# Kernel tuning notes

Hardware: AMD Instinct MI355X
Metric: run time of the kernel (lower is better)

Reference implementation:

```python
import jax, jax.numpy as jnp
import numpy as np

H = 512  # hidden_size
D = 512  # input_size
EPS = 1e-5  # torch LayerNorm default


def _ln(u, g, b):
    # LayerNorm over last dim, biased variance (matches torch)
    m = jnp.mean(u, axis=-1, keepdims=True)
    v = jnp.mean(jnp.square(u - m), axis=-1, keepdims=True)
    return (u - m) * jax.lax.rsqrt(v + EPS) * g + b


def _cell(x_t, h, c, W, b, ln_g, ln_b):
    # gates: [B, 4H] from concat([x_t, h]) @ W.T + b
    z = jnp.concatenate([x_t, h], axis=-1) @ W.T + b
    i_raw, f_raw, g_raw, o_raw = jnp.split(z, 4, axis=-1)
    i = jax.nn.sigmoid(_ln(i_raw, ln_g[0], ln_b[0]))
    f = jax.nn.sigmoid(_ln(f_raw, ln_g[1], ln_b[1]))
    g = jnp.tanh(_ln(g_raw, ln_g[2], ln_b[2]))
    o = jax.nn.sigmoid(_ln(o_raw, ln_g[3], ln_b[3]))
    c_new = f * c + i * g
    h_new = o * jnp.tanh(_ln(c_new, ln_g[4], ln_b[4]))
    return h_new, c_new


def setup_inputs() -> dict:
    key = jax.random.key(0)
    ks = jax.random.split(key, 5)
    B, T = 64, 1024
    x = jax.random.normal(ks[0], (B, T, D), dtype=jnp.float32)
    W0 = jax.random.normal(ks[1], (4 * H, D + H), dtype=jnp.float32) * 0.02
    b0 = jnp.zeros((4 * H,), jnp.float32)
    W1 = jax.random.normal(ks[2], (4 * H, H + H), dtype=jnp.float32) * 0.02
    b1 = jnp.zeros((4 * H,), jnp.float32)
    ln_g0 = jnp.ones((5, H), jnp.float32)
    ln_b0 = jnp.zeros((5, H), jnp.float32)
    ln_g1 = jnp.ones((5, H), jnp.float32)
    ln_b1 = jnp.zeros((5, H), jnp.float32)
    hw_W = jax.random.normal(ks[3], (H, H), dtype=jnp.float32) * 0.02
    hw_b = jnp.zeros((H,), jnp.float32)
    return {"x": x, "W0": W0, "b0": b0, "ln_g0": ln_g0, "ln_b0": ln_b0,
            "W1": W1, "b1": b1, "ln_g1": ln_g1, "ln_b1": ln_b1,
            "hw_W": hw_W, "hw_b": hw_b}


def reference(x, W0, b0, ln_g0, ln_b0, W1, b1, ln_g1, ln_b1, hw_W, hw_b):
    B, T, _ = x.shape
    h0 = jnp.zeros((B, H), x.dtype)
    c0 = jnp.zeros((B, H), x.dtype)
    h1 = jnp.zeros((B, H), x.dtype)
    c1 = jnp.zeros((B, H), x.dtype)

    def step(carry, x_t):
        h0, c0, h1, c1 = carry
        h0n, c0n = _cell(x_t, h0, c0, W0, b0, ln_g0, ln_b0)
        # dropout=0.0 -> identity between layers
        h1n, c1n = _cell(h0n, h1, c1, W1, b1, ln_g1, ln_b1)
        # highway: gate computed from h_in (= layer-0 output)
        g = jax.nn.sigmoid(h0n @ hw_W.T + hw_b)
        out_t = g * h1n + (1.0 - g) * h0n
        return (h0n, c0n, h1n, c1n), out_t

    xs = jnp.transpose(x, (1, 0, 2))  # [T, B, D]
    (h0, c0, h1, c1), outs = jax.lax.scan(step, (h0, c0, h1, c1), xs)
    output = jnp.transpose(outs, (1, 0, 2))  # [B, T, H]
    h_n = jnp.stack([h0, h1], axis=0)  # [num_layers, B, H]
    c_n = jnp.stack([c0, c1], axis=0)
    return output, h_n, c_n
```

## Files before the change

### kernel.cpp

```cpp
#include <hip/hip_runtime.h>

#define TT 1024
#define BB 64
#define HH 512
#define DD 512
#define NBLK 256
#define NTHR 256
#define NGRP 8

#define W0T4_OFF 0
#define W1T4_OFF 2097152
#define H0_OFF   4194304
#define H1_OFF   4227072
#define Z0_OFF   4259840
#define Z1_OFF   4390912
#define HWZ_OFF  4521984
#define FLG_OFF  4554752

__device__ __forceinline__ float ldg_cg(const float* p) {
    return __hip_atomic_load(p, __ATOMIC_RELAXED, __HIP_MEMORY_SCOPE_AGENT);
}
__device__ __forceinline__ void stg_cg(float* p, float v) {
    __hip_atomic_store(p, v, __ATOMIC_RELAXED, __HIP_MEMORY_SCOPE_AGENT);
}
__device__ __forceinline__ float4 ldg_cg4(const float* p) {
    const unsigned long long* q = (const unsigned long long*)p;
    unsigned long long a = __hip_atomic_load(q,     __ATOMIC_RELAXED, __HIP_MEMORY_SCOPE_AGENT);
    unsigned long long b = __hip_atomic_load(q + 1, __ATOMIC_RELAXED, __HIP_MEMORY_SCOPE_AGENT);
    float4 v;
    ((unsigned long long*)&v)[0] = a;
    ((unsigned long long*)&v)[1] = b;
    return v;
}
__device__ __forceinline__ unsigned ldg_cgu(const unsigned* p) {
    return __hip_atomic_load(p, __ATOMIC_RELAXED, __HIP_MEMORY_SCOPE_AGENT);
}

__device__ __forceinline__ void group_barrier(unsigned* gfl, unsigned tgt, int slot, int tid)
{
    __syncthreads();
    if (tid == 0)
        __hip_atomic_store(&gfl[slot * 32], tgt, __ATOMIC_RELEASE, __HIP_MEMORY_SCOPE_AGENT);
    if (tid < 32) {
        while (ldg_cgu(&gfl[tid * 32]) < tgt) __builtin_amdgcn_s_sleep(1);
    }
    __syncthreads();
}

__global__ void ln_lstm_init_kernel(const float* __restrict__ W0, const float* __restrict__ W1,
                                    float* __restrict__ ws)
{
    const int stride = gridDim.x * blockDim.x;
    const int idx = blockIdx.x * blockDim.x + threadIdx.x;
    for (int i = idx; i < 2048 * 256; i += stride) {
        const int R = i & 2047, kq = i >> 11;
        const float4 v0 = *(const float4*)&W0[(size_t)R * 1024 + kq * 4];
        const float4 v1 = *(const float4*)&W1[(size_t)R * 1024 + kq * 4];
        *(float4*)&ws[W0T4_OFF + ((size_t)kq * 2048 + R) * 4] = v0;
        *(float4*)&ws[W1T4_OFF + ((size_t)kq * 2048 + R) * 4] = v1;
    }
    for (int i = idx; i < 65536; i += stride) ws[H0_OFF + i] = 0.f;
    unsigned* uw = (unsigned*)ws;
    for (int i = idx; i < 8192; i += stride) uw[FLG_OFF + i] = 0u;
}

__device__ __forceinline__ void gemv_k4(const float4* __restrict__ wt, const float* __restrict__ inT,
                                        float* __restrict__ zr, int bq, int r, int Rrow,
                                        float& z0, float& z1)
{
    float a[8];
#pragma unroll
    for (int i = 0; i < 8; ++i) a[i] = 0.f;
    const float4* wp = wt + (size_t)(bq * 64) * 2048 + Rrow;
    const float* ib = inT + bq * 256;
    for (int c = 0; c < 4; ++c) {
        float4 w[16];
#pragma unroll
        for (int i = 0; i < 16; ++i) w[i] = wp[(size_t)(c * 16 + i) * 2048];
#pragma unroll
        for (int i = 0; i < 16; ++i) {
            const int kk = c * 64 + i * 4;
#pragma unroll
            for (int bi = 0; bi < 8; ++bi) {
                const float4 iv = *(const float4*)&ib[bi * 1024 + kk];
                a[bi] += w[i].x * iv.x + w[i].y * iv.y + w[i].z * iv.z + w[i].w * iv.w;
            }
        }
    }
#pragma unroll
    for (int bi = 0; bi < 8; ++bi) zr[bq * 512 + bi * 64 + r] = a[bi];
    __syncthreads();
    z0 = 0.f; z1 = 0.f;
#pragma unroll
    for (int w2 = 0; w2 < 4; ++w2) {
        z0 += zr[w2 * 512 + bq * 64 + r];
        z1 += zr[w2 * 512 + (bq + 4) * 64 + r];
    }
}

__device__ __forceinline__ void block_reduce8(float v[8], float* sred, int tid)
{
#pragma unroll
    for (int off = 32; off > 0; off >>= 1)
#pragma unroll
        for (int k = 0; k < 8; ++k) v[k] += __shfl_down(v[k], off, 64);
    __syncthreads();
    if ((tid & 63) == 0) {
        const int wv = tid >> 6;
#pragma unroll
        for (int k = 0; k < 8; ++k) sred[k * 4 + wv] = v[k];
    }
    __syncthreads();
#pragma unroll
    for (int k = 0; k < 8; ++k)
        v[k] = sred[k * 4 + 0] + sred[k * 4 + 1] + sred[k * 4 + 2] + sred[k * 4 + 3];
}
__device__ __forceinline__ void block_reduce2(float& s1, float& s2, float* sred, int tid)
{
#pragma unroll
    for (int off = 32; off > 0; off >>= 1) {
        s1 += __shfl_down(s1, off, 64);
        s2 += __shfl_down(s2, off, 64);
    }
    __syncthreads();
    if ((tid & 63) == 0) {
        const int wv = tid >> 6;
        sred[wv] = s1; sred[4 + wv] = s2;
    }
    __syncthreads();
    s1 = sred[0] + sred[1] + sred[2] + sred[3];
    s2 = sred[4] + sred[5] + sred[6] + sred[7];
}

__device__ __forceinline__ void cell(const float* __restrict__ zg, const float* __restrict__ gb,
                                     const float* __restrict__ lng, const float* __restrict__ lnb,
                                     float cc[2], float* __restrict__ hws_b, float hv[2],
                                     float* sred, int tid)
{
    float z[4][2];
#pragma unroll
    for (int g = 0; g < 4; ++g) {
        z[g][0] = ldg_cg(zg + g * 512 + tid)       + gb[g * 512 + tid];
        z[g][1] = ldg_cg(zg + g * 512 + tid + 256) + gb[g * 512 + tid + 256];
    }
    float st[8];
#pragma unroll
    for (int g = 0; g < 4; ++g) {
        st[g]     = z[g][0] + z[g][1];
        st[4 + g] = z[g][0] * z[g][0] + z[g][1] * z[g][1];
    }
    block_reduce8(st, sred, tid);
    float act[4][2];
#pragma unroll
    for (int g = 0; g < 4; ++g) {
        const float mu = st[g] * (1.f / 512.f);
        const float rs = rsqrtf(st[4 + g] * (1.f / 512.f) - mu * mu + 1e-5f);
#pragma unroll
        for (int e = 0; e < 2; ++e) {
            const int j = tid + e * 256;
            const float a = (z[g][e] - mu) * rs * lng[g * 512 + j] + lnb[g * 512 + j];
            act[g][e] = (g == 2) ? tanhf(a) : 1.f / (1.f + expf(-a));
        }
    }
    float cn[2];
#pragma unroll
    for (int e = 0; e < 2; ++e) {
        cn[e] = act[1][e] * cc[e] + act[0][e] * act[2][e];
        cc[e] = cn[e];
    }
    float s1 = cn[0] + cn[1];
    float s2 = cn[0] * cn[0] + cn[1] * cn[1];
    block_reduce2(s1, s2, sred, tid);
    const float mu = s1 * (1.f / 512.f);
    const float rs = rsqrtf(s2 * (1.f / 512.f) - mu * mu + 1e-5f);
#pragma unroll
    for (int e = 0; e < 2; ++e) {
        const int j = tid + e * 256;
        const float h = act[3][e] * tanhf((cn[e] - mu) * rs * lng[2048 + j] + lnb[2048 + j]);
        stg_cg(hws_b + j, h);
        hv[e] = h;
    }
}

__global__ __launch_bounds__(NTHR, 1)
void LayerNormLSTMStack_55508157333865_kernel(
    const float* __restrict__ x,
    const float* __restrict__ W0, const float* __restrict__ gb0,
    const float* __restrict__ lng0, const float* __restrict__ lnb0,
    const float* __restrict__ W1, const float* __restrict__ gb1,
    const float* __restrict__ lng1, const float* __restrict__ lnb1,
    const float* __restrict__ hwW, const float* __restrict__ hwb,
    float* __restrict__ out, float* __restrict__ ws)
{
    __shared__ __align__(16) float inT[8 * 1024];
    __shared__ __align__(16) float zr[4 * 512];
    __shared__ float sred[32];
    __shared__ float hwred[256];

    const int tid = threadIdx.x;
    const int grp = blockIdx.x >> 5;
    const int bg  = blockIdx.x & 31;
    const int bb0 = grp * 8;
    const int r = tid & 63, bq = tid >> 6;
    const int R0 = bg * 64;

    const float4* w0t = (const float4*)(ws + W0T4_OFF);
    const float4* w1t = (const float4*)(ws + W1T4_OFF);
    float* h0ws  = ws + H0_OFF;
    float* h1ws  = ws + H1_OFF;
    float* z0g   = ws + Z0_OFF + grp * 16384;
    float* z1g   = ws + Z1_OFF + grp * 16384;
    float* hwzg  = ws + HWZ_OFF + grp * 4096;
    unsigned* gfl = (unsigned*)ws + FLG_OFF + grp * 1024;

    float c0[2] = {0.f, 0.f}, c1[2] = {0.f, 0.f};
    unsigned ph = 0;
    const size_t OUT_SZ = (size_t)BB * TT * HH;

    for (int t = 0; t < TT; ++t) {
        const int sbi = tid >> 5, part = tid & 31;

        {
            const float* xp = x + ((size_t)(bb0 + sbi) * TT + t) * DD + part * 16;
            float* d = &inT[sbi * 1024 + part * 16];
            *(float4*)(d)      = *(const float4*)(xp);
            *(float4*)(d + 4)  = *(const float4*)(xp + 4);
            *(float4*)(d + 8)  = *(const float4*)(xp + 8);
            *(float4*)(d + 12) = *(const float4*)(xp + 12);
            const float* hp = h0ws + (size_t)(bb0 + sbi) * 512 + part * 16;
            float* dh = &inT[sbi * 1024 + 512 + part * 16];
            *(float4*)(dh)      = ldg_cg4(hp);
            *(float4*)(dh + 4)  = ldg_cg4(hp + 4);
            *(float4*)(dh + 8)  = ldg_cg4(hp + 8);
            *(float4*)(dh + 12) = ldg_cg4(hp + 12);
        }
        __syncthreads();
        {
            float z0, z1;
            gemv_k4(w0t, inT, zr, bq, r, R0 + r, z0, z1);
            stg_cg(z0g + (size_t)bq * 2048 + R0 + r, z0);
            stg_cg(z0g + (size_t)(bq + 4) * 2048 + R0 + r, z1);
        }
        group_barrier(gfl, ++ph, bg, tid);

        if (bg < 8) {
            const int b = bb0 + bg;
            float hv0[2];
            cell(z0g + (size_t)bg * 2048, gb0, lng0, lnb0, c0, h0ws + (size_t)b * 512, hv0, sred, tid);
            if (t == TT - 1) {
#pragma unroll
                for (int e = 0; e < 2; ++e) {
                    const int j = tid + e * 256;
                    out[OUT_SZ + (size_t)b * 512 + j]         = hv0[e];
                    out[OUT_SZ + 65536 + (size_t)b * 512 + j] = c0[e];
                }
            }
        }
        group_barrier(gfl, ++ph, bg, tid);

        {
            const float* hp0 = h0ws + (size_t)(bb0 + sbi) * 512 + part * 16;
            float* d0 = &inT[sbi * 1024 + part * 16];
            *(float4*)(d0)      = ldg_cg4(hp0);
            *(float4*)(d0 + 4)  = ldg_cg4(hp0 + 4);
            *(float4*)(d0 + 8)  = ldg_cg4(hp0 + 8);
            *(float4*)(d0 + 12) = ldg_cg4(hp0 + 12);
            const float* hp1 = h1ws + (size_t)(bb0 + sbi) * 512 + part * 16;
            float* dh = &inT[sbi * 1024 + 512 + part * 16];
            *(float4*)(dh)      = ldg_cg4(hp1);
            *(float4*)(dh + 4)  = ldg_cg4(hp1 + 4);
            *(float4*)(dh + 8)  = ldg_cg4(hp1 + 8);
            *(float4*)(dh + 12) = ldg_cg4(hp1 + 12);
        }
        __syncthreads();
        {
            float z0, z1;
            gemv_k4(w1t, inT, zr, bq, r, R0 + r, z0, z1);
            stg_cg(z1g + (size_t)bq * 2048 + R0 + r, z0);
            stg_cg(z1g + (size_t)(bq + 4) * 2048 + R0 + r, z1);
        }
        {
            const int rh = tid & 15, bi = (tid >> 4) & 7, hf = tid >> 7;
            const float* wr = hwW + (size_t)(bg * 16 + rh) * 512 + hf * 256;
            const float* ibh = &inT[bi * 1024 + hf * 256];
            float acc = 0.f;
#pragma unroll 8
            for (int k = 0; k < 256; k += 4) {
                const float4 wv = *(const float4*)&wr[k];
                const float4 iv = *(const float4*)&ibh[k];
                acc += wv.x * iv.x + wv.y * iv.y + wv.z * iv.z + wv.w * iv.w;
            }
            hwred[tid] = acc;
            __syncthreads();
            if (tid < 128)
                stg_cg(hwzg + (size_t)bi * 512 + bg * 16 + rh, hwred[tid] + hwred[tid + 128]);
        }
        group_barrier(gfl, ++ph, bg, tid);

        if (bg < 8) {
            const int b = bb0 + bg;
            float hv1[2];
            cell(z1g + (size_t)bg * 2048, gb1, lng1, lnb1, c1, h1ws + (size_t)b * 512, hv1, sred, tid);
#pragma unroll
            for (int e = 0; e < 2; ++e) {
                const int j = tid + e * 256;
                const float hz = ldg_cg(hwzg + (size_t)bg * 512 + j) + hwb[j];
                const float gt = 1.f / (1.f + expf(-hz));
                const float h0v = ldg_cg(h0ws + (size_t)b * 512 + j);
                out[((size_t)b * TT + t) * HH + j] = gt * hv1[e] + (1.f - gt) * h0v;
            }
            if (t == TT - 1) {
#pragma unroll
                for (int e = 0; e < 2; ++e) {
                    const int j = tid + e * 256;
                    out[OUT_SZ + 32768 + (size_t)b * 512 + j] = hv1[e];
                    out[OUT_SZ + 98304 + (size_t)b * 512 + j] = c1[e];
                }
            }
        }
        group_barrier(gfl, ++ph, bg, tid);
    }
}

extern "C" void kernel_launch(void* const* d_in, const int* in_sizes, int n_in,
                              void* d_out, int out_size, void* d_ws, size_t ws_size,
                              hipStream_t stream)
{
    (void)in_sizes; (void)n_in; (void)out_size; (void)ws_size;
    const float* x    = (const float*)d_in[0];
    const float* W0   = (const float*)d_in[1];
    const float* b0   = (const float*)d_in[2];
    const float* lng0 = (const float*)d_in[3];
    const float* lnb0 = (const float*)d_in[4];
    const float* W1   = (const float*)d_in[5];
    const float* b1   = (const float*)d_in[6];
    const float* lng1 = (const float*)d_in[7];
    const float* lnb1 = (const float*)d_in[8];
    const float* hwW  = (const float*)d_in[9];
    const float* hwb  = (const float*)d_in[10];
    float* out = (float*)d_out;
    float* ws  = (float*)d_ws;

    ln_lstm_init_kernel<<<dim3(256), dim3(256), 0, stream>>>(W0, W1, ws);
    LayerNormLSTMStack_55508157333865_kernel<<<dim3(NBLK), dim3(NTHR), 0, stream>>>(
        x, W0, b0, lng0, lnb0, W1, b1, lng1, lnb1, hwW, hwb, out, ws);
}
```

Baseline: 60.10 ms.

## Software-pipeline layer-0 step t+1 with layer-1 step t to halve group barriers

Restructures the time loop so the layer-0 gate GEMV for step t+1 runs in the same phase as the layer-1 GEMV and highway projection for step t. The layer-0 cell for t+1 then runs right after the layer-1 cell, cutting per-step group barriers from four to two. h0 is reused from shared memory and kept in registers rather than reloaded from global memory. The highway bias loads are hoisted out of the loop. The change adds a prologue, extra __syncthreads and more work per phase, and it depends on careful reuse of the shared input buffer.

```diff
diff --git a/kernel.cpp b/kernel.cpp
--- a/kernel.cpp
+++ b/kernel.cpp
@@ -214,49 +214,39 @@
     unsigned* gfl = (unsigned*)ws + FLG_OFF + grp * 1024;
 
     float c0[2] = {0.f, 0.f}, c1[2] = {0.f, 0.f};
+    float hv0[2] = {0.f, 0.f};
     unsigned ph = 0;
     const size_t OUT_SZ = (size_t)BB * TT * HH;
+    const int sbi = tid >> 5, part = tid & 31;
+    const float hwb0 = hwb[tid], hwb1 = hwb[tid + 256];
+
+    {
+        const float* xp = x + ((size_t)(bb0 + sbi) * TT + 0) * DD + part * 16;
+        float* d = &inT[sbi * 1024 + part * 16];
+        *(float4*)(d)      = *(const float4*)(xp);
+        *(float4*)(d + 4)  = *(const float4*)(xp + 4);
+        *(float4*)(d + 8)  = *(const float4*)(xp + 8);
+        *(float4*)(d + 12) = *(const float4*)(xp + 12);
+        float* dh = &inT[sbi * 1024 + 512 + part * 16];
+        *(float4*)(dh) = make_float4(0.f, 0.f, 0.f, 0.f);
+        *(float4*)(dh + 4) = make_float4(0.f, 0.f, 0.f, 0.f);
+        *(float4*)(dh + 8) = make_float4(0.f, 0.f, 0.f, 0.f);
+        *(float4*)(dh + 12) = make_float4(0.f, 0.f, 0.f, 0.f);
+    }
+    __syncthreads();
+    {
+        float z0, z1;
+        gemv_k4(w0t, inT, zr, bq, r, R0 + r, z0, z1);
+        stg_cg(z0g + (size_t)bq * 2048 + R0 + r, z0);
+        stg_cg(z0g + (size_t)(bq + 4) * 2048 + R0 + r, z1);
+    }
+    group_barrier(gfl, ++ph, bg, tid);
+    if (bg < 8)
+        cell(z0g + (size_t)bg * 2048, gb0, lng0, lnb0, c0, h0ws + (size_t)(bb0 + bg) * 512, hv0, sred, tid);
+    group_barrier(gfl, ++ph, bg, tid);
 
     for (int t = 0; t < TT; ++t) {
-        const int sbi = tid >> 5, part = tid & 31;
-
-        {
-            const float* xp = x + ((size_t)(bb0 + sbi) * TT + t) * DD + part * 16;
-            float* d = &inT[sbi * 1024 + part * 16];
-            *(float4*)(d)      = *(const float4*)(xp);
-            *(float4*)(d + 4)  = *(const float4*)(xp + 4);
-            *(float4*)(d + 8)  = *(const float4*)(xp + 8);
-            *(float4*)(d + 12) = *(const float4*)(xp + 12);
-            const float* hp = h0ws + (size_t)(bb0 + sbi) * 512 + part * 16;
-            float* dh = &inT[sbi * 1024 + 512 + part * 16];
-            *(float4*)(dh)      = ldg_cg4(hp);
-            *(float4*)(dh + 4)  = ldg_cg4(hp + 4);
-            *(float4*)(dh + 8)  = ldg_cg4(hp + 8);
-            *(float4*)(dh + 12) = ldg_cg4(hp + 12);
-        }
-        __syncthreads();
-        {
-            float z0, z1;
-            gemv_k4(w0t, inT, zr, bq, r, R0 + r, z0, z1);
-            stg_cg(z0g + (size_t)bq * 2048 + R0 + r, z0);
-            stg_cg(z0g + (size_t)(bq + 4) * 2048 + R0 + r, z1);
-        }
-        group_barrier(gfl, ++ph, bg, tid);
-
-        if (bg < 8) {
-            const int b = bb0 + bg;
-            float hv0[2];
-            cell(z0g + (size_t)bg * 2048, gb0, lng0, lnb0, c0, h0ws + (size_t)b * 512, hv0, sred, tid);
-            if (t == TT - 1) {
-#pragma unroll
-                for (int e = 0; e < 2; ++e) {
-                    const int j = tid + e * 256;
-                    out[OUT_SZ + (size_t)b * 512 + j]         = hv0[e];
-                    out[OUT_SZ + 65536 + (size_t)b * 512 + j] = c0[e];
-                }
-            }
-        }
-        group_barrier(gfl, ++ph, bg, tid);
+        const bool more = (t + 1 < TT);
 
         {
             const float* hp0 = h0ws + (size_t)(bb0 + sbi) * 512 + part * 16;
@@ -295,26 +285,63 @@
             if (tid < 128)
                 stg_cg(hwzg + (size_t)bi * 512 + bg * 16 + rh, hwred[tid] + hwred[tid + 128]);
         }
+        if (more) {
+            float4 h0a, h0b, h0c, h0d;
+            {
+                const float* src = &inT[sbi * 1024 + part * 16];
+                h0a = *(const float4*)(src);
+                h0b = *(const float4*)(src + 4);
+                h0c = *(const float4*)(src + 8);
+                h0d = *(const float4*)(src + 12);
+            }
+            const float* xp = x + ((size_t)(bb0 + sbi) * TT + (t + 1)) * DD + part * 16;
+            const float4 xa = *(const float4*)(xp);
+            const float4 xb = *(const float4*)(xp + 4);
+            const float4 xc = *(const float4*)(xp + 8);
+            const float4 xd = *(const float4*)(xp + 12);
+            __syncthreads();
+            {
+                float* dh = &inT[sbi * 1024 + 512 + part * 16];
+                *(float4*)(dh)      = h0a;
+                *(float4*)(dh + 4)  = h0b;
+                *(float4*)(dh + 8)  = h0c;
+                *(float4*)(dh + 12) = h0d;
+                float* d0 = &inT[sbi * 1024 + part * 16];
+                *(float4*)(d0)      = xa;
+                *(float4*)(d0 + 4)  = xb;
+                *(float4*)(d0 + 8)  = xc;
+                *(float4*)(d0 + 12) = xd;
+            }
+            __syncthreads();
+            float z0, z1;
+            gemv_k4(w0t, inT, zr, bq, r, R0 + r, z0, z1);
+            stg_cg(z0g + (size_t)bq * 2048 + R0 + r, z0);
+            stg_cg(z0g + (size_t)(bq + 4) * 2048 + R0 + r, z1);
+        }
         group_barrier(gfl, ++ph, bg, tid);
 
         if (bg < 8) {
             const int b = bb0 + bg;
             float hv1[2];
             cell(z1g + (size_t)bg * 2048, gb1, lng1, lnb1, c1, h1ws + (size_t)b * 512, hv1, sred, tid);
-#pragma unroll
-            for (int e = 0; e < 2; ++e) {
-                const int j = tid + e * 256;
-                const float hz = ldg_cg(hwzg + (size_t)bg * 512 + j) + hwb[j];
-                const float gt = 1.f / (1.f + expf(-hz));
-                const float h0v = ldg_cg(h0ws + (size_t)b * 512 + j);
-                out[((size_t)b * TT + t) * HH + j] = gt * hv1[e] + (1.f - gt) * h0v;
-            }
-            if (t == TT - 1) {
+            {
+                const float hz0 = ldg_cg(hwzg + (size_t)bg * 512 + tid) + hwb0;
+                const float hz1 = ldg_cg(hwzg + (size_t)bg * 512 + tid + 256) + hwb1;
+                const float gt0 = 1.f / (1.f + expf(-hz0));
+                const float gt1 = 1.f / (1.f + expf(-hz1));
+                out[((size_t)b * TT + t) * HH + tid]       = gt0 * hv1[0] + (1.f - gt0) * hv0[0];
+                out[((size_t)b * TT + t) * HH + tid + 256] = gt1 * hv1[1] + (1.f - gt1) * hv0[1];
+            }
+            if (more) {
+                cell(z0g + (size_t)bg * 2048, gb0, lng0, lnb0, c0, h0ws + (size_t)b * 512, hv0, sred, tid);
+            } else {
 #pragma unroll
                 for (int e = 0; e < 2; ++e) {
                     const int j = tid + e * 256;
-                    out[OUT_SZ + 32768 + (size_t)b * 512 + j] = hv1[e];
-                    out[OUT_SZ + 98304 + (size_t)b * 512 + j] = c1[e];
+                    out[OUT_SZ + (size_t)b * 512 + j]          = hv0[e];
+                    out[OUT_SZ + 32768 + (size_t)b * 512 + j]  = hv1[e];
+                    out[OUT_SZ + 65536 + (size_t)b * 512 + j]  = c0[e];
+                    out[OUT_SZ + 98304 + (size_t)b * 512 + j]  = c1[e];
                 }
             }
         }
```

Result: faster. 51.92 ms (-13.6%).

## Skew layer-0 step t+1 into layer-1 phase and double threads per block

Applied to the files above, without the earlier changes.

Restructures the per-timestep schedule so the layer-0 GEMV for step t+1 runs in the same phase as the layer-1 and highway GEMVs for step t, and the layer-0 cell for t+1 runs right after the layer-1 cell. This cuts group barriers per timestep from four to two, removing cross-block synchronisation latency from the serial recurrence. It also doubles the block to 512 threads, splitting K eight ways so each thread handles one hidden element in the cell. That adds shared-memory reduction work and register pressure, and the prologue and last-step handling must be exactly right.

```diff
diff --git a/kernel.cpp b/kernel.cpp
--- a/kernel.cpp
+++ b/kernel.cpp
@@ -5,7 +5,7 @@
 #define HH 512
 #define DD 512
 #define NBLK 256
-#define NTHR 256
+#define NTHR 512
 #define NGRP 8
 
 #define W0T4_OFF 0
@@ -64,16 +64,17 @@
     for (int i = idx; i < 8192; i += stride) uw[FLG_OFF + i] = 0u;
 }
 
-__device__ __forceinline__ void gemv_k4(const float4* __restrict__ wt, const float* __restrict__ inT,
+__device__ __forceinline__ void gemv_k8(const float4* __restrict__ wt, const float* __restrict__ inT,
                                         float* __restrict__ zr, int bq, int r, int Rrow,
-                                        float& z0, float& z1)
+                                        int bi_out, float& z)
 {
     float a[8];
 #pragma unroll
     for (int i = 0; i < 8; ++i) a[i] = 0.f;
-    const float4* wp = wt + (size_t)(bq * 64) * 2048 + Rrow;
-    const float* ib = inT + bq * 256;
-    for (int c = 0; c < 4; ++c) {
+    const float4* wp = wt + (size_t)(bq * 32) * 2048 + Rrow;
+    const float* ib = inT + bq * 128;
+#pragma unroll
+    for (int c = 0; c < 2; ++c) {
         float4 w[16];
 #pragma unroll
         for (int i = 0; i < 16; ++i) w[i] = wp[(size_t)(c * 16 + i) * 2048];
@@ -90,12 +91,9 @@
 #pragma unroll
     for (int bi = 0; bi < 8; ++bi) zr[bq * 512 + bi * 64 + r] = a[bi];
     __syncthreads();
-    z0 = 0.f; z1 = 0.f;
-#pragma unroll
-    for (int w2 = 0; w2 < 4; ++w2) {
-        z0 += zr[w2 * 512 + bq * 64 + r];
-        z1 += zr[w2 * 512 + (bq + 4) * 64 + r];
-    }
+    z = 0.f;
+#pragma unroll
+    for (int w2 = 0; w2 < 8; ++w2) z += zr[w2 * 512 + bi_out * 64 + r];
 }
 
 __device__ __forceinline__ void block_reduce8(float v[8], float* sred, int tid)
@@ -108,12 +106,16 @@
     if ((tid & 63) == 0) {
         const int wv = tid >> 6;
 #pragma unroll
-        for (int k = 0; k < 8; ++k) sred[k * 4 + wv] = v[k];
-    }
-    __syncthreads();
-#pragma unroll
-    for (int k = 0; k < 8; ++k)
-        v[k] = sred[k * 4 + 0] + sred[k * 4 + 1] + sred[k * 4 + 2] + sred[k * 4 + 3];
+        for (int k = 0; k < 8; ++k) sred[k * 8 + wv] = v[k];
+    }
+    __syncthreads();
+#pragma unroll
+    for (int k = 0; k < 8; ++k) {
+        float s = 0.f;
+#pragma unroll
+        for (int i = 0; i < 8; ++i) s += sred[k * 8 + i];
+        v[k] = s;
+    }
 }
 __device__ __forceinline__ void block_reduce2(float& s1, float& s2, float* sred, int tid)
 {
@@ -125,61 +127,44 @@
     __syncthreads();
     if ((tid & 63) == 0) {
         const int wv = tid >> 6;
-        sred[wv] = s1; sred[4 + wv] = s2;
-    }
-    __syncthreads();
-    s1 = sred[0] + sred[1] + sred[2] + sred[3];
-    s2 = sred[4] + sred[5] + sred[6] + sred[7];
+        sred[wv] = s1; sred[8 + wv] = s2;
+    }
+    __syncthreads();
+    s1 = 0.f; s2 = 0.f;
+#pragma unroll
+    for (int i = 0; i < 8; ++i) { s1 += sred[i]; s2 += sred[8 + i]; }
 }
 
 __device__ __forceinline__ void cell(const float* __restrict__ zg, const float* __restrict__ gb,
                                      const float* __restrict__ lng, const float* __restrict__ lnb,
-                                     float cc[2], float* __restrict__ hws_b, float hv[2],
+                                     float& cc, float* __restrict__ hws_b, float& hv,
                                      float* sred, int tid)
 {
-    float z[4][2];
-#pragma unroll
-    for (int g = 0; g < 4; ++g) {
-        z[g][0] = ldg_cg(zg + g * 512 + tid)       + gb[g * 512 + tid];
-        z[g][1] = ldg_cg(zg + g * 512 + tid + 256) + gb[g * 512 + tid + 256];
-    }
+    float z[4];
+#pragma unroll
+    for (int g = 0; g < 4; ++g)
+        z[g] = ldg_cg(zg + g * 512 + tid) + gb[g * 512 + tid];
     float st[8];
 #pragma unroll
-    for (int g = 0; g < 4; ++g) {
-        st[g]     = z[g][0] + z[g][1];
-        st[4 + g] = z[g][0] * z[g][0] + z[g][1] * z[g][1];
-    }
+    for (int g = 0; g < 4; ++g) { st[g] = z[g]; st[4 + g] = z[g] * z[g]; }
     block_reduce8(st, sred, tid);
-    float act[4][2];
+    float act[4];
 #pragma unroll
     for (int g = 0; g < 4; ++g) {
         const float mu = st[g] * (1.f / 512.f);
         const float rs = rsqrtf(st[4 + g] * (1.f / 512.f) - mu * mu + 1e-5f);
-#pragma unroll
-        for (int e = 0; e < 2; ++e) {
-            const int j = tid + e * 256;
-            const float a = (z[g][e] - mu) * rs * lng[g * 512 + j] + lnb[g * 512 + j];
-            act[g][e] = (g == 2) ? tanhf(a) : 1.f / (1.f + expf(-a));
-        }
-    }
-    float cn[2];
-#pragma unroll
-    for (int e = 0; e < 2; ++e) {
-        cn[e] = act[1][e] * cc[e] + act[0][e] * act[2][e];
-        cc[e] = cn[e];
-    }
-    float s1 = cn[0] + cn[1];
-    float s2 = cn[0] * cn[0] + cn[1] * cn[1];
+        const float a = (z[g] - mu) * rs * lng[g * 512 + tid] + lnb[g * 512 + tid];
+        act[g] = (g == 2) ? tanhf(a) : 1.f / (1.f + expf(-a));
+    }
+    const float cn = act[1] * cc + act[0] * act[2];
+    cc = cn;
+    float s1 = cn, s2 = cn * cn;
     block_reduce2(s1, s2, sred, tid);
     const float mu = s1 * (1.f / 512.f);
     const float rs = rsqrtf(s2 * (1.f / 512.f) - mu * mu + 1e-5f);
-#pragma unroll
-    for (int e = 0; e < 2; ++e) {
-        const int j = tid + e * 256;
-        const float h = act[3][e] * tanhf((cn[e] - mu) * rs * lng[2048 + j] + lnb[2048 + j]);
-        stg_cg(hws_b + j, h);
-        hv[e] = h;
-    }
+    const float h = act[3] * tanhf((cn - mu) * rs * lng[2048 + tid] + lnb[2048 + tid]);
+    stg_cg(hws_b + tid, h);
+    hv = h;
 }
 
 __global__ __launch_bounds__(NTHR, 1)
@@ -193,9 +178,9 @@
     float* __restrict__ out, float* __restrict__ ws)
 {
     __shared__ __align__(16) float inT[8 * 1024];
-    __shared__ __align__(16) float zr[4 * 512];
-    __shared__ float sred[32];
-    __shared__ float hwred[256];
+    __shared__ __align__(16) float zr[8 * 512];
+    __shared__ float sred[64];
+    __shared__ float hwred[512];
 
     const int tid = threadIdx.x;
     const int grp = blockIdx.x >> 5;
@@ -213,79 +198,57 @@
     float* hwzg  = ws + HWZ_OFF + grp * 4096;
     unsigned* gfl = (unsigned*)ws + FLG_OFF + grp * 1024;
 
-    float c0[2] = {0.f, 0.f}, c1[2] = {0.f, 0.f};
+    float c0 = 0.f, c1 = 0.f;
+    float hv0 = 0.f;
     unsigned ph = 0;
     const size_t OUT_SZ = (size_t)BB * TT * HH;
+    const int sbi = tid >> 6, part = tid & 63;
+    const float hwb_r = hwb[tid];
+
+    {
+        const float* xp = x + ((size_t)(bb0 + sbi) * TT + 0) * DD;
+        float* d = &inT[sbi * 1024];
+        *(float4*)&d[part * 4]       = *(const float4*)&xp[part * 4];
+        *(float4*)&d[256 + part * 4] = *(const float4*)&xp[256 + part * 4];
+        *(float4*)&d[512 + part * 4] = make_float4(0.f, 0.f, 0.f, 0.f);
+        *(float4*)&d[768 + part * 4] = make_float4(0.f, 0.f, 0.f, 0.f);
+    }
+    __syncthreads();
+    {
+        float z;
+        gemv_k8(w0t, inT, zr, bq, r, R0 + r, bq, z);
+        stg_cg(z0g + (size_t)bq * 2048 + R0 + r, z);
+    }
+    group_barrier(gfl, ++ph, bg, tid);
+    if (bg < 8)
+        cell(z0g + (size_t)bg * 2048, gb0, lng0, lnb0, c0, h0ws + (size_t)(bb0 + bg) * 512, hv0, sred, tid);
+    group_barrier(gfl, ++ph, bg, tid);
 
     for (int t = 0; t < TT; ++t) {
-        const int sbi = tid >> 5, part = tid & 31;
+        const bool more = (t + 1 < TT);
 
         {
-            const float* xp = x + ((size_t)(bb0 + sbi) * TT + t) * DD + part * 16;
-            float* d = &inT[sbi * 1024 + part * 16];
-            *(float4*)(d)      = *(const float4*)(xp);
-            *(float4*)(d + 4)  = *(const float4*)(xp + 4);
-            *(float4*)(d + 8)  = *(const float4*)(xp + 8);
-            *(float4*)(d + 12) = *(const float4*)(xp + 12);
-            const float* hp = h0ws + (size_t)(bb0 + sbi) * 512 + part * 16;
-            float* dh = &inT[sbi * 1024 + 512 + part * 16];
-            *(float4*)(dh)      = ldg_cg4(hp);
-            *(float4*)(dh + 4)  = ldg_cg4(hp + 4);
-            *(float4*)(dh + 8)  = ldg_cg4(hp + 8);
-            *(float4*)(dh + 12) = ldg_cg4(hp + 12);
+            const float* hp0 = h0ws + (size_t)(bb0 + sbi) * 512;
+            float* d = &inT[sbi * 1024];
+            *(float4*)&d[part * 4]       = ldg_cg4(hp0 + part * 4);
+            *(float4*)&d[256 + part * 4] = ldg_cg4(hp0 + 256 + part * 4);
+            const float* hp1 = h1ws + (size_t)(bb0 + sbi) * 512;
+            *(float4*)&d[512 + part * 4] = ldg_cg4(hp1 + part * 4);
+            *(float4*)&d[768 + part * 4] = ldg_cg4(hp1 + 256 + part * 4);
         }
         __syncthreads();
         {
-            float z0, z1;
-            gemv_k4(w0t, inT, zr, bq, r, R0 + r, z0, z1);
-            stg_cg(z0g + (size_t)bq * 2048 + R0 + r, z0);
-            stg_cg(z0g + (size_t)(bq + 4) * 2048 + R0 + r, z1);
-        }
-        group_barrier(gfl, ++ph, bg, tid);
-
-        if (bg < 8) {
-            const int b = bb0 + bg;
-            float hv0[2];
-            cell(z0g + (size_t)bg * 2048, gb0, lng0, lnb0, c0, h0ws + (size_t)b * 512, hv0, sred, tid);
-            if (t == TT - 1) {
-#pragma unroll
-                for (int e = 0; e < 2; ++e) {
-                    const int j = tid + e * 256;
-                    out[OUT_SZ + (size_t)b * 512 + j]         = hv0[e];
-                    out[OUT_SZ + 65536 + (size_t)b * 512 + j] = c0[e];
-                }
-            }
-        }
-        group_barrier(gfl, ++ph, bg, tid);
-
+            float z;
+            gemv_k8(w1t, inT, zr, bq, r, R0 + r, bq, z);
+            stg_cg(z1g + (size_t)bq * 2048 + R0 + r, z);
+        }
         {
-            const float* hp0 = h0ws + (size_t)(bb0 + sbi) * 512 + part * 16;
-            float* d0 = &inT[sbi * 1024 + part * 16];
-            *(float4*)(d0)      = ldg_cg4(hp0);
-            *(float4*)(d0 + 4)  = ldg_cg4(hp0 + 4);
-            *(float4*)(d0 + 8)  = ldg_cg4(hp0 + 8);
-            *(float4*)(d0 + 12) = ldg_cg4(hp0 + 12);
-            const float* hp1 = h1ws + (size_t)(bb0 + sbi) * 512 + part * 16;
-            float* dh = &inT[sbi * 1024 + 512 + part * 16];
-            *(float4*)(dh)      = ldg_cg4(hp1);
-            *(float4*)(dh + 4)  = ldg_cg4(hp1 + 4);
-            *(float4*)(dh + 8)  = ldg_cg4(hp1 + 8);
-            *(float4*)(dh + 12) = ldg_cg4(hp1 + 12);
-        }
-        __syncthreads();
-        {
-            float z0, z1;
-            gemv_k4(w1t, inT, zr, bq, r, R0 + r, z0, z1);
-            stg_cg(z1g + (size_t)bq * 2048 + R0 + r, z0);
-            stg_cg(z1g + (size_t)(bq + 4) * 2048 + R0 + r, z1);
-        }
-        {
-            const int rh = tid & 15, bi = (tid >> 4) & 7, hf = tid >> 7;
-            const float* wr = hwW + (size_t)(bg * 16 + rh) * 512 + hf * 256;
-            const float* ibh = &inT[bi * 1024 + hf * 256];
+            const int rh = tid & 15, bi = (tid >> 4) & 7, qk = tid >> 7;
+            const float* wr = hwW + (size_t)(bg * 16 + rh) * 512 + qk * 128;
+            const float* ibh = &inT[bi * 1024 + qk * 128];
             float acc = 0.f;
 #pragma unroll 8
-            for (int k = 0; k < 256; k += 4) {
+            for (int k = 0; k < 128; k += 4) {
                 const float4 wv = *(const float4*)&wr[k];
                 const float4 iv = *(const float4*)&ibh[k];
                 acc += wv.x * iv.x + wv.y * iv.y + wv.z * iv.z + wv.w * iv.w;
@@ -293,29 +256,50 @@
             hwred[tid] = acc;
             __syncthreads();
             if (tid < 128)
-                stg_cg(hwzg + (size_t)bi * 512 + bg * 16 + rh, hwred[tid] + hwred[tid + 128]);
+                stg_cg(hwzg + (size_t)((tid >> 4) & 7) * 512 + bg * 16 + (tid & 15),
+                       hwred[tid] + hwred[tid + 128] + hwred[tid + 256] + hwred[tid + 384]);
+        }
+        if (more) {
+            float4 h0a, h0b;
+            {
+                const float* src = &inT[sbi * 1024];
+                h0a = *(const float4*)&src[part * 4];
+                h0b = *(const float4*)&src[256 + part * 4];
+            }
+            const float* xp = x + ((size_t)(bb0 + sbi) * TT + (t + 1)) * DD;
+            const float4 xa = *(const float4*)&xp[part * 4];
+            const float4 xb = *(const float4*)&xp[256 + part * 4];
+            __syncthreads();
+            {
+                float* d = &inT[sbi * 1024];
+                *(float4*)&d[512 + part * 4] = h0a;
+                *(float4*)&d[768 + part * 4] = h0b;
+                *(float4*)&d[part * 4]       = xa;
+                *(float4*)&d[256 + part * 4] = xb;
+            }
+            __syncthreads();
+            float z;
+            gemv_k8(w0t, inT, zr, bq, r, R0 + r, bq, z);
+            stg_cg(z0g + (size_t)bq * 2048 + R0 + r, z);
         }
         group_barrier(gfl, ++ph, bg, tid);
 
         if (bg < 8) {
             const int b = bb0 + bg;
-            float hv1[2];
+            float hv1;
             cell(z1g + (size_t)bg * 2048, gb1, lng1, lnb1, c1, h1ws + (size_t)b * 512, hv1, sred, tid);
-#pragma unroll
-            for (int e = 0; e < 2; ++e) {
-                const int j = tid + e * 256;
-                const float hz = ldg_cg(hwzg + (size_t)bg * 512 + j) + hwb[j];
+            {
+                const float hz = ldg_cg(hwzg + (size_t)bg * 512 + tid) + hwb_r;
                 const float gt = 1.f / (1.f + expf(-hz));
-                const float h0v = ldg_cg(h0ws + (size_t)b * 512 + j);
-                out[((size_t)b * TT + t) * HH + j] = gt * hv1[e] + (1.f - gt) * h0v;
-            }
-            if (t == TT - 1) {
-#pragma unroll
-                for (int e = 0; e < 2; ++e) {
-                    const int j = tid + e * 256;
-                    out[OUT_SZ + 32768 + (size_t)b * 512 + j] = hv1[e];
-                    out[OUT_SZ + 98304 + (size_t)b * 512 + j] = c1[e];
-                }
+                out[((size_t)b * TT + t) * HH + tid] = gt * hv1 + (1.f - gt) * hv0;
+            }
+            if (more) {
+                cell(z0g + (size_t)bg * 2048, gb0, lng0, lnb0, c0, h0ws + (size_t)b * 512, hv0, sred, tid);
+            } else {
+                out[OUT_SZ + (size_t)b * 512 + tid]         = hv0;
+                out[OUT_SZ + 32768 + (size_t)b * 512 + tid] = hv1;
+                out[OUT_SZ + 65536 + (size_t)b * 512 + tid] = c0;
+                out[OUT_SZ + 98304 + (size_t)b * 512 + tid] = c1;
             }
         }
         group_barrier(gfl, ++ph, bg, tid);
```

After: 56.69 ms. -5.7%, faster.

## Software-pipeline layer-0 step t+1 with layer-1 step t to halve group barriers

Applied to the files above, without the earlier changes.

Each timestep now loads x[t+1], h0[t] and h1[t-1] into one shared buffer and computes the layer-1 GEMV, the highway GEMV and the next layer-0 GEMV before a single barrier. Layer-0 and layer-1 cells then run concurrently on different blocks of the group. This cuts the per-step group barriers from four to two and removes one global h0 reload. The h0 value for the highway mix is read from shared memory. Stores change to system-scope atomics, which may cost more per store.

```diff
diff --git a/kernel.cpp b/kernel.cpp
--- a/kernel.cpp
+++ b/kernel.cpp
@@ -7,6 +7,7 @@
 #define NBLK 256
 #define NTHR 256
 #define NGRP 8
+#define BSTR 1536
 
 #define W0T4_OFF 0
 #define W1T4_OFF 2097152
@@ -20,9 +21,6 @@
 __device__ __forceinline__ float ldg_cg(const float* p) {
     return __hip_atomic_load(p, __ATOMIC_RELAXED, __HIP_MEMORY_SCOPE_AGENT);
 }
-__device__ __forceinline__ void stg_cg(float* p, float v) {
-    __hip_atomic_store(p, v, __ATOMIC_RELAXED, __HIP_MEMORY_SCOPE_AGENT);
-}
 __device__ __forceinline__ float4 ldg_cg4(const float* p) {
     const unsigned long long* q = (const unsigned long long*)p;
     unsigned long long a = __hip_atomic_load(q,     __ATOMIC_RELAXED, __HIP_MEMORY_SCOPE_AGENT);
@@ -35,6 +33,9 @@
 __device__ __forceinline__ unsigned ldg_cgu(const unsigned* p) {
     return __hip_atomic_load(p, __ATOMIC_RELAXED, __HIP_MEMORY_SCOPE_AGENT);
 }
+__device__ __forceinline__ void stg_wt(float* p, float v) {
+    __hip_atomic_store(p, v, __ATOMIC_RELAXED, __HIP_MEMORY_SCOPE_SYSTEM);
+}
 
 __device__ __forceinline__ void group_barrier(unsigned* gfl, unsigned tgt, int slot, int tid)
 {
@@ -64,15 +65,15 @@
     for (int i = idx; i < 8192; i += stride) uw[FLG_OFF + i] = 0u;
 }
 
-__device__ __forceinline__ void gemv_k4(const float4* __restrict__ wt, const float* __restrict__ inT,
-                                        float* __restrict__ zr, int bq, int r, int Rrow,
-                                        float& z0, float& z1)
+__device__ __forceinline__ void gemv_k4u(const float4* __restrict__ wt, const float* __restrict__ inT,
+                                         int koff, float* __restrict__ zr, int bq, int r, int Rrow,
+                                         float& z0, float& z1)
 {
     float a[8];
 #pragma unroll
     for (int i = 0; i < 8; ++i) a[i] = 0.f;
     const float4* wp = wt + (size_t)(bq * 64) * 2048 + Rrow;
-    const float* ib = inT + bq * 256;
+    const float* ib = inT + koff + bq * 256;
     for (int c = 0; c < 4; ++c) {
         float4 w[16];
 #pragma unroll
@@ -82,7 +83,7 @@
             const int kk = c * 64 + i * 4;
 #pragma unroll
             for (int bi = 0; bi < 8; ++bi) {
-                const float4 iv = *(const float4*)&ib[bi * 1024 + kk];
+                const float4 iv = *(const float4*)&ib[bi * BSTR + kk];
                 a[bi] += w[i].x * iv.x + w[i].y * iv.y + w[i].z * iv.z + w[i].w * iv.w;
             }
         }
@@ -177,7 +178,7 @@
     for (int e = 0; e < 2; ++e) {
         const int j = tid + e * 256;
         const float h = act[3][e] * tanhf((cn[e] - mu) * rs * lng[2048 + j] + lnb[2048 + j]);
-        stg_cg(hws_b + j, h);
+        stg_wt(hws_b + j, h);
         hv[e] = h;
     }
 }
@@ -192,7 +193,7 @@
     const float* __restrict__ hwW, const float* __restrict__ hwb,
     float* __restrict__ out, float* __restrict__ ws)
 {
-    __shared__ __align__(16) float inT[8 * 1024];
+    __shared__ __align__(16) float inT[8 * BSTR];
     __shared__ __align__(16) float zr[4 * 512];
     __shared__ float sred[32];
     __shared__ float hwred[256];
@@ -214,75 +215,75 @@
     unsigned* gfl = (unsigned*)ws + FLG_OFF + grp * 1024;
 
     float c0[2] = {0.f, 0.f}, c1[2] = {0.f, 0.f};
+    float hv0[2] = {0.f, 0.f};
     unsigned ph = 0;
     const size_t OUT_SZ = (size_t)BB * TT * HH;
+    const int sbi = tid >> 5, part = tid & 31;
+
+    {
+        const float* xp = x + ((size_t)(bb0 + sbi) * TT + 0) * DD + part * 16;
+        float* d = &inT[sbi * BSTR + part * 16];
+        *(float4*)(d)      = *(const float4*)(xp);
+        *(float4*)(d + 4)  = *(const float4*)(xp + 4);
+        *(float4*)(d + 8)  = *(const float4*)(xp + 8);
+        *(float4*)(d + 12) = *(const float4*)(xp + 12);
+        float* dh = &inT[sbi * BSTR + 512 + part * 16];
+        const float4 zz = make_float4(0.f, 0.f, 0.f, 0.f);
+        *(float4*)(dh) = zz; *(float4*)(dh + 4) = zz; *(float4*)(dh + 8) = zz; *(float4*)(dh + 12) = zz;
+    }
+    __syncthreads();
+    {
+        float z0, z1;
+        gemv_k4u(w0t, inT, 0, zr, bq, r, R0 + r, z0, z1);
+        stg_wt(z0g + (size_t)bq * 2048 + R0 + r, z0);
+        stg_wt(z0g + (size_t)(bq + 4) * 2048 + R0 + r, z1);
+    }
+    group_barrier(gfl, ++ph, bg, tid);
+    if (bg < 8)
+        cell(z0g + (size_t)bg * 2048, gb0, lng0, lnb0, c0, h0ws + (size_t)(bb0 + bg) * 512, hv0, sred, tid);
+    group_barrier(gfl, ++ph, bg, tid);
 
     for (int t = 0; t < TT; ++t) {
-        const int sbi = tid >> 5, part = tid & 31;
+        const bool more = (t + 1 < TT);
+        const int tx = more ? (t + 1) : (TT - 1);
 
         {
-            const float* xp = x + ((size_t)(bb0 + sbi) * TT + t) * DD + part * 16;
-            float* d = &inT[sbi * 1024 + part * 16];
-            *(float4*)(d)      = *(const float4*)(xp);
-            *(float4*)(d + 4)  = *(const float4*)(xp + 4);
-            *(float4*)(d + 8)  = *(const float4*)(xp + 8);
-            *(float4*)(d + 12) = *(const float4*)(xp + 12);
-            const float* hp = h0ws + (size_t)(bb0 + sbi) * 512 + part * 16;
-            float* dh = &inT[sbi * 1024 + 512 + part * 16];
-            *(float4*)(dh)      = ldg_cg4(hp);
-            *(float4*)(dh + 4)  = ldg_cg4(hp + 4);
-            *(float4*)(dh + 8)  = ldg_cg4(hp + 8);
-            *(float4*)(dh + 12) = ldg_cg4(hp + 12);
+            const float* xp = x + ((size_t)(bb0 + sbi) * TT + tx) * DD + part * 16;
+            const float4 xa = *(const float4*)(xp);
+            const float4 xb = *(const float4*)(xp + 4);
+            const float4 xc = *(const float4*)(xp + 8);
+            const float4 xd = *(const float4*)(xp + 12);
+            const float* hp0 = h0ws + (size_t)(bb0 + sbi) * 512 + part * 16;
+            const float4 h0a = ldg_cg4(hp0);
+            const float4 h0b = ldg_cg4(hp0 + 4);
+            const float4 h0c = ldg_cg4(hp0 + 8);
+            const float4 h0d = ldg_cg4(hp0 + 12);
+            const float* hp1 = h1ws + (size_t)(bb0 + sbi) * 512 + part * 16;
+            const float4 h1a = ldg_cg4(hp1);
+            const float4 h1b = ldg_cg4(hp1 + 4);
+            const float4 h1c = ldg_cg4(hp1 + 8);
+            const float4 h1d = ldg_cg4(hp1 + 12);
+            float* d = &inT[sbi * BSTR + part * 16];
+            *(float4*)(d)      = xa; *(float4*)(d + 4)  = xb;
+            *(float4*)(d + 8)  = xc; *(float4*)(d + 12) = xd;
+            float* dh0 = &inT[sbi * BSTR + 512 + part * 16];
+            *(float4*)(dh0)      = h0a; *(float4*)(dh0 + 4)  = h0b;
+            *(float4*)(dh0 + 8)  = h0c; *(float4*)(dh0 + 12) = h0d;
+            float* dh1 = &inT[sbi * BSTR + 1024 + part * 16];
+            *(float4*)(dh1)      = h1a; *(float4*)(dh1 + 4)  = h1b;
+            *(float4*)(dh1 + 8)  = h1c; *(float4*)(dh1 + 12) = h1d;
         }
         __syncthreads();
         {
             float z0, z1;
-            gemv_k4(w0t, inT, zr, bq, r, R0 + r, z0, z1);
-            stg_cg(z0g + (size_t)bq * 2048 + R0 + r, z0);
-            stg_cg(z0g + (size_t)(bq + 4) * 2048 + R0 + r, z1);
-        }
-        group_barrier(gfl, ++ph, bg, tid);
-
-        if (bg < 8) {
-            const int b = bb0 + bg;
-            float hv0[2];
-            cell(z0g + (size_t)bg * 2048, gb0, lng0, lnb0, c0, h0ws + (size_t)b * 512, hv0, sred, tid);
-            if (t == TT - 1) {
-#pragma unroll
-                for (int e = 0; e < 2; ++e) {
-                    const int j = tid + e * 256;
-                    out[OUT_SZ + (size_t)b * 512 + j]         = hv0[e];
-                    out[OUT_SZ + 65536 + (size_t)b * 512 + j] = c0[e];
-                }
-            }
-        }
-        group_barrier(gfl, ++ph, bg, tid);
-
-        {
-            const float* hp0 = h0ws + (size_t)(bb0 + sbi) * 512 + part * 16;
-            float* d0 = &inT[sbi * 1024 + part * 16];
-            *(float4*)(d0)      = ldg_cg4(hp0);
-            *(float4*)(d0 + 4)  = ldg_cg4(hp0 + 4);
-            *(float4*)(d0 + 8)  = ldg_cg4(hp0 + 8);
-            *(float4*)(d0 + 12) = ldg_cg4(hp0 + 12);
-            const float* hp1 = h1ws + (size_t)(bb0 + sbi) * 512 + part * 16;
-            float* dh = &inT[sbi * 1024 + 512 + part * 16];
-            *(float4*)(dh)      = ldg_cg4(hp1);
-            *(float4*)(dh + 4)  = ldg_cg4(hp1 + 4);
-            *(float4*)(dh + 8)  = ldg_cg4(hp1 + 8);
-            *(float4*)(dh + 12) = ldg_cg4(hp1 + 12);
-        }
-        __syncthreads();
-        {
-            float z0, z1;
-            gemv_k4(w1t, inT, zr, bq, r, R0 + r, z0, z1);
-            stg_cg(z1g + (size_t)bq * 2048 + R0 + r, z0);
-            stg_cg(z1g + (size_t)(bq + 4) * 2048 + R0 + r, z1);
+            gemv_k4u(w1t, inT, 512, zr, bq, r, R0 + r, z0, z1);
+            stg_wt(z1g + (size_t)bq * 2048 + R0 + r, z0);
+            stg_wt(z1g + (size_t)(bq + 4) * 2048 + R0 + r, z1);
         }
         {
             const int rh = tid & 15, bi = (tid >> 4) & 7, hf = tid >> 7;
             const float* wr = hwW + (size_t)(bg * 16 + rh) * 512 + hf * 256;
-            const float* ibh = &inT[bi * 1024 + hf * 256];
+            const float* ibh = &inT[bi * BSTR + 512 + hf * 256];
             float acc = 0.f;
 #pragma unroll 8
             for (int k = 0; k < 256; k += 4) {
@@ -293,23 +294,43 @@
             hwred[tid] = acc;
             __syncthreads();
             if (tid < 128)
-                stg_cg(hwzg + (size_t)bi * 512 + bg * 16 + rh, hwred[tid] + hwred[tid + 128]);
+                stg_wt(hwzg + (size_t)((tid >> 4) & 7) * 512 + bg * 16 + (tid & 15),
+                       hwred[tid] + hwred[tid + 128]);
+        }
+        if (more) {
+            float z0, z1;
+            gemv_k4u(w0t, inT, 0, zr, bq, r, R0 + r, z0, z1);
+            stg_wt(z0g + (size_t)bq * 2048 + R0 + r, z0);
+            stg_wt(z0g + (size_t)(bq + 4) * 2048 + R0 + r, z1);
         }
         group_barrier(gfl, ++ph, bg, tid);
 
         if (bg < 8) {
             const int b = bb0 + bg;
+            if (more) {
+                cell(z0g + (size_t)bg * 2048, gb0, lng0, lnb0, c0, h0ws + (size_t)b * 512, hv0, sred, tid);
+            } else {
+#pragma unroll
+                for (int e = 0; e < 2; ++e) {
+                    const int j = tid + e * 256;
+                    out[OUT_SZ + (size_t)b * 512 + j]         = hv0[e];
+                    out[OUT_SZ + 65536 + (size_t)b * 512 + j] = c0[e];
+                }
+            }
+        } else if (bg < 16) {
+            const int bi = bg - 8;
+            const int b = bb0 + bi;
             float hv1[2];
-            cell(z1g + (size_t)bg * 2048, gb1, lng1, lnb1, c1, h1ws + (size_t)b * 512, hv1, sred, tid);
+            cell(z1g + (size_t)bi * 2048, gb1, lng1, lnb1, c1, h1ws + (size_t)b * 512, hv1, sred, tid);
 #pragma unroll
             for (int e = 0; e < 2; ++e) {
                 const int j = tid + e * 256;
-                const float hz = ldg_cg(hwzg + (size_t)bg * 512 + j) + hwb[j];
+                const float hz = ldg_cg(hwzg + (size_t)bi * 512 + j) + hwb[j];
                 const float gt = 1.f / (1.f + expf(-hz));
-                const float h0v = ldg_cg(h0ws + (size_t)b * 512 + j);
+                const float h0v = inT[bi * BSTR + 512 + j];
                 out[((size_t)b * TT + t) * HH + j] = gt * hv1[e] + (1.f - gt) * h0v;
             }
-            if (t == TT - 1) {
+            if (!more) {
 #pragma unroll
                 for (int e = 0; e < 2; ++e) {
                     const int j = tid + e * 256;
```

Result: faster. 50.06 ms (-16.7%).
